# Kernel tuning notes

Measured on AMD Instinct MI355X. Metric: run time of the kernel, lower is better.

The kernel has to match this reference:

```python
import jax, jax.numpy as jnp
import numpy as np
from jax import lax

EPS = 1e-5  # BatchNorm eps (torch default)

def _up2_bilinear_ac(x):
    # bilinear upsample x2, align_corners=True; x: [B,C,H,W]
    B, C, H, W = x.shape
    def axis_interp(n_in, n_out):
        pos = jnp.arange(n_out, dtype=jnp.float32) * ((n_in - 1) / (n_out - 1))
        i0 = jnp.floor(pos).astype(jnp.int32)
        i1 = jnp.minimum(i0 + 1, n_in - 1)
        w = (pos - i0.astype(jnp.float32)).astype(x.dtype)
        return i0, i1, w
    i0, i1, wh = axis_interp(H, 2 * H)
    x = x[:, :, i0, :] * (1.0 - wh)[None, None, :, None] + x[:, :, i1, :] * wh[None, None, :, None]
    j0, j1, ww = axis_interp(W, 2 * W)
    x = x[:, :, :, j0] * (1.0 - ww) + x[:, :, :, j1] * ww
    return x

def setup_inputs() -> dict:
    key = jax.random.key(0)
    ks = jax.random.split(key, 8)
    B, Cin, Cout, H, W = 8, 64, 32, 128, 128
    att, K = 16, 2  # attention_channel = max(int(64*0.0625),16)=16; kernel_num=2
    n = lambda k, s, sc: jax.random.normal(k, s, jnp.float32) * sc
    return {
        'x': n(ks[0], (B, Cin, H, W), 1.0),
        'fc_w': n(ks[1], (att, Cin), 0.1),
        'bn_a_gamma': jnp.ones((att,), jnp.float32), 'bn_a_beta': jnp.zeros((att,), jnp.float32),
        'bn_a_mean': jnp.zeros((att,), jnp.float32), 'bn_a_var': jnp.ones((att,), jnp.float32),
        'ch_w': n(ks[2], (Cin, att), 0.1), 'ch_b': jnp.zeros((Cin,), jnp.float32),
        'fil_w': n(ks[3], (Cout, att), 0.1), 'fil_b': jnp.zeros((Cout,), jnp.float32),
        'sp_w': n(ks[4], (9, att), 0.1), 'sp_b': jnp.zeros((9,), jnp.float32),
        'k_w': n(ks[5], (K, att), 0.1), 'k_b': jnp.zeros((K,), jnp.float32),
        'weight': n(ks[6], (K, Cout, Cin, 3, 3), 0.05),
        'bn_gamma': jnp.ones((Cout,), jnp.float32), 'bn_beta': jnp.zeros((Cout,), jnp.float32),
        'bn_mean': jnp.zeros((Cout,), jnp.float32), 'bn_var': jnp.ones((Cout,), jnp.float32),
    }

def reference(x, fc_w, bn_a_gamma, bn_a_beta, bn_a_mean, bn_a_var,
              ch_w, ch_b, fil_w, fil_b, sp_w, sp_b, k_w, k_b,
              weight, bn_gamma, bn_beta, bn_mean, bn_var):
    x = _up2_bilinear_ac(x)
    B, Cin, H, W = x.shape
    K, Cout = weight.shape[0], weight.shape[1]
    # --- ODConv attention branch (on GAP features) ---
    g = x.mean(axis=(2, 3))                                    # [B,Cin]
    h = g @ fc_w.T                                             # [B,att]
    h = (h - bn_a_mean) / jnp.sqrt(bn_a_var + EPS) * bn_a_gamma + bn_a_beta
    h = jax.nn.relu(h)
    ch_att = jax.nn.sigmoid(h @ ch_w.T + ch_b)                 # [B,Cin]
    fil_att = jax.nn.sigmoid(h @ fil_w.T + fil_b)              # [B,Cout]
    sp_att = jax.nn.sigmoid(h @ sp_w.T + sp_b).reshape(B, 1, 1, 1, 3, 3)
    k_att = jax.nn.softmax(h @ k_w.T + k_b, axis=1).reshape(B, K, 1, 1, 1, 1)
    # per-sample aggregated filters: [B,Cout,Cin,3,3]
    agg_w = jnp.sum(k_att * sp_att * weight[None], axis=1)
    # --- dynamic conv (per-sample filter), channel-attended input ---
    x = x * ch_att[:, :, None, None]
    def conv1(xi, wi):
        return lax.conv_general_dilated(xi[None], wi, (1, 1), [(1, 1), (1, 1)],
                                        dimension_numbers=('NCHW', 'OIHW', 'NCHW'))[0]
    y = jax.vmap(conv1)(x, agg_w)                              # [B,Cout,H,W]
    y = y * fil_att[:, :, None, None]
    # --- BatchNorm2d (inference) + GELU (exact erf) ---
    y = (y - bn_mean[:, None, None]) / jnp.sqrt(bn_var[:, None, None] + EPS)
    y = y * bn_gamma[:, None, None] + bn_beta[:, None, None]
    return jax.nn.gelu(y, approximate=False)
```

## Files before the change

kernel.cpp:

```cpp
#include <hip/hip_runtime.h>
#include <hip/hip_bf16.h>

#define EPSBN 1e-5f

typedef short short8 __attribute__((ext_vector_type(8)));
typedef float f32x16 __attribute__((ext_vector_type(16)));

static __device__ __forceinline__ unsigned short f2u(float f){
  __hip_bfloat16 h = __float2bfloat16(f);
  union { __hip_bfloat16 h; unsigned short u; } c; c.h = h; return c.u;
}

#define WS_G     2048
#define WS_S     7168
#define WS_T     8192
#define WS_AGGB  16384
#define WS_XUP   327680

__global__ __launch_bounds__(256) void k_gap(const float* __restrict__ x, float* __restrict__ g){
  __shared__ float w[128];
  __shared__ float partial[4];
  int tid = threadIdx.x;
  if (tid < 128){
    int i = tid;
    float s = 0.f;
    int rstart = max(0, (int)floorf((float)(i-1)*(255.0f/127.0f)));
    #pragma unroll
    for (int k = 0; k < 8; ++k){
      int r = rstart + k;
      if (r <= 255){
        float pos = (float)r * (127.0f/255.0f);
        int i0 = (int)pos; float fr = pos - (float)i0; int i1 = min(i0+1,127);
        if (i0 == i) s += 1.0f - fr;
        if (i1 == i) s += fr;
      }
    }
    w[i] = s;
  }
  __syncthreads();
  const float4* xp = (const float4*)(x + ((size_t)blockIdx.x << 14));
  float s = 0.f;
  for (int gi = tid; gi < 4096; gi += 256){
    int i = gi >> 5, j4 = (gi & 31) * 4;
    float4 v = xp[gi];
    s += (v.x*w[j4] + v.y*w[j4+1] + v.z*w[j4+2] + v.w*w[j4+3]) * w[i];
  }
  for (int off = 32; off > 0; off >>= 1) s += __shfl_down(s, off, 64);
  if ((tid & 63) == 0) partial[tid >> 6] = s;
  __syncthreads();
  if (tid == 0) g[blockIdx.x] = (partial[0]+partial[1]+partial[2]+partial[3]) * (1.0f/65536.0f);
}

__global__ __launch_bounds__(256) void k_aggw(const float* __restrict__ g,
                      const float* __restrict__ fc_w,
                      const float* __restrict__ bga, const float* __restrict__ bba,
                      const float* __restrict__ bma, const float* __restrict__ bva,
                      const float* __restrict__ ch_w, const float* __restrict__ ch_b,
                      const float* __restrict__ fil_w, const float* __restrict__ fil_b,
                      const float* __restrict__ sp_w, const float* __restrict__ sp_b,
                      const float* __restrict__ k_w, const float* __restrict__ k_b,
                      const float* __restrict__ bn_g, const float* __restrict__ bn_b,
                      const float* __restrict__ bn_m, const float* __restrict__ bn_v,
                      const float* __restrict__ weight,
                      unsigned short* __restrict__ aggb,
                      float* __restrict__ sS, float* __restrict__ tT)
{
  __shared__ float h[8][16];
  int tid = threadIdx.x;
  if (tid < 128){
    int b = tid >> 4, a = tid & 15;
    float acc = 0.f;
    for (int c = 0; c < 64; ++c) acc += g[b*64+c] * fc_w[a*64+c];
    float v = (acc - bma[a]) * rsqrtf(bva[a] + EPSBN) * bga[a] + bba[a];
    h[b][a] = fmaxf(v, 0.f);
  }
  __syncthreads();

  int idx = blockIdx.x*256 + tid;
  int ci_l = idx & 31;
  int o    = (idx >> 5) & 31;
  int s    = (idx >> 10) % 9;
  int t2   = (idx >> 10) / 9;
  int cc   = t2 & 1, b = t2 >> 1;
  int ci   = cc*32 + ci_l;

  const float* hb = h[b];
  float zc = ch_b[ci], zs = sp_b[s];
  float z0 = k_b[0],  z1 = k_b[1];
  #pragma unroll
  for (int a = 0; a < 16; ++a){
    float hv = hb[a];
    zc += hv*ch_w[ci*16+a];
    zs += hv*sp_w[s*16+a];
    z0 += hv*k_w[a];
    z1 += hv*k_w[16+a];
  }
  float chv = 1.f/(1.f+expf(-zc));
  float spv = 1.f/(1.f+expf(-zs));
  float m = fmaxf(z0,z1);
  float e0 = expf(z0-m), e1 = expf(z1-m), inv = 1.f/(e0+e1);
  float ka0 = e0*inv, ka1 = e1*inv;
  float w0 = weight[(o*64+ci)*9+s];
  float w1 = weight[((32+o)*64+ci)*9+s];
  aggb[idx] = f2u(chv*spv*(ka0*w0 + ka1*w1));

  if (blockIdx.x == 0){
    int bb = tid >> 5, oo = tid & 31;
    float z = fil_b[oo];
    #pragma unroll
    for (int a = 0; a < 16; ++a) z += h[bb][a]*fil_w[oo*16+a];
    float f = 1.f/(1.f+expf(-z));
    float invs = rsqrtf(bn_v[oo] + EPSBN);
    sS[tid] = f * bn_g[oo] * invs;
    if (bb == 0) tT[oo] = bn_b[oo] - bn_m[oo]*bn_g[oo]*invs;
  }
}

__global__ __launch_bounds__(256) void k_up(const float* __restrict__ x,
                                            unsigned int* __restrict__ xup32)
{
  __shared__ float xin[16*798];
  int tid = threadIdx.x;
  int bi  = blockIdx.x;
  int strip = bi & 31, h16 = (bi >> 5) & 3, b = bi >> 7;
  int r0 = strip * 8;
  int i0b = (int)((float)r0 * (127.0f/255.0f));

  for (int e = tid; e < 12288; e += 256){
    int ir = e >> 11, rem = e & 2047, ci = rem >> 7, j = rem & 127;
    int row = min(i0b + ir, 127);
    xin[ci*798 + ir*133 + j] = x[(((size_t)(b*64 + h16*16 + ci)) << 14) + (row << 7) + j];
  }
  __syncthreads();

  int ci2 = tid & 7, cbase = tid >> 3;
  int j0t[8], j1t[8]; float wwt[8];
  #pragma unroll
  for (int jj = 0; jj < 8; ++jj){
    int c = cbase + 32*jj;
    float pos = (float)c * (127.0f/255.0f);
    int j0 = (int)pos;
    j0t[jj] = j0; j1t[jj] = min(j0+1,127); wwt[jj] = pos - (float)j0;
  }
  const float* base0 = &xin[(ci2*2+0)*798];
  const float* base1 = &xin[(ci2*2+1)*798];
  size_t pxbase = ((size_t)(b*2 + (h16>>1))) << 16;
  int halfoff = (h16 & 1)*8;

  for (int rr = 0; rr < 8; ++rr){
    int r = r0 + rr;
    float posr = (float)r * (127.0f/255.0f);
    int i0 = (int)posr; float wh = posr - (float)i0;
    int ir0 = (i0 - i0b)*133, ir1 = (min(i0+1,127) - i0b)*133;
    #pragma unroll
    for (int jj = 0; jj < 8; ++jj){
      int c = cbase + 32*jj;
      int j0 = j0t[jj], j1 = j1t[jj]; float ww = wwt[jj];
      float v00 = base0[ir0+j0], v01 = base0[ir0+j1];
      float v10 = base0[ir1+j0], v11 = base0[ir1+j1];
      float a0 = v00 + (v01-v00)*ww;
      float a1 = v10 + (v11-v10)*ww;
      float r0v = a0 + (a1-a0)*wh;
      float u00 = base1[ir0+j0], u01 = base1[ir0+j1];
      float u10 = base1[ir1+j0], u11 = base1[ir1+j1];
      float b0 = u00 + (u01-u00)*ww;
      float b1 = u10 + (u11-u10)*ww;
      float r1v = b0 + (b1-b0)*wh;
      unsigned pack = (unsigned)f2u(r0v) | (((unsigned)f2u(r1v)) << 16);
      xup32[(pxbase + (size_t)(r*256 + c))*16 + halfoff + ci2] = pack;
    }
  }
}

#define XT_STRIDE 40
__global__ __launch_bounds__(256) void k_conv(const unsigned short* __restrict__ xup,
                                              const unsigned short* __restrict__ aggb,
                                              const float* __restrict__ sS,
                                              const float* __restrict__ tT,
                                              float* __restrict__ out)
{
  __shared__ unsigned short xt[18*18*XT_STRIDE];
  __shared__ unsigned short wt[288*XT_STRIDE];
  __shared__ float sSs[32], tTs[32];

  int tid = threadIdx.x;
  int bi  = blockIdx.x;
  int b   = bi >> 8, t = bi & 255;
  int p0  = (t >> 4) * 16, q0 = (t & 15) * 16;
  int lane = tid & 63, wv = tid >> 6;
  if (tid < 32){ sSs[tid] = sS[b*32+tid]; tTs[tid] = tT[tid]; }

  int ldsoff[6], gmoff[6]; bool val[6];
  int cnt = (tid < 16) ? 6 : 5;
  for (int k = 0; k < cnt; ++k){
    int e = tid + (k << 8);
    int rr = e / 72; int rem = e - rr*72; int qq = rem >> 2; int gq4 = rem & 3;
    int gr = p0 - 1 + rr, gq = q0 - 1 + qq;
    val[k]    = ((unsigned)gr < 256u) && ((unsigned)gq < 256u);
    ldsoff[k] = (rr*18+qq)*XT_STRIDE + gq4*8;
    gmoff[k]  = (gr*256+gq)*32 + gq4*8;
  }

  f32x16 acc[2];
  #pragma unroll
  for (int i = 0; i < 16; ++i){ acc[0][i] = 0.f; acc[1][i] = 0.f; }

  int n  = lane & 31;
  int kq = lane >> 5;

  for (int cc = 0; cc < 2; ++cc){
    if (cc) __syncthreads();
    const unsigned short* xb = xup + (((size_t)(b*2+cc)) << 21);
    for (int k = 0; k < cnt; ++k){
      short8 v = {0,0,0,0,0,0,0,0};
      if (val[k]) v = *(const short8*)&xb[gmoff[k]];
      *(short8*)&xt[ldsoff[k]] = v;
    }
    const unsigned short* wbg = aggb + ((size_t)(b*2+cc))*9216;
    for (int e = tid; e < 1152; e += 256){
      *(short8*)&wt[(e >> 2)*XT_STRIDE + (e & 3)*8] = *(const short8*)&wbg[e*8];
    }
    __syncthreads();

    #pragma unroll
    for (int s = 0; s < 9; ++s){
      const int ky = s / 3, kx = s % 3;
      #pragma unroll
      for (int k2 = 0; k2 < 2; ++k2){
        short8 av = *(const short8*)&wt[(s*32 + n)*XT_STRIDE + k2*16 + kq*8];
        #pragma unroll
        for (int tt = 0; tt < 2; ++tt){
          int lr = 2*(2*wv + tt) + (n >> 4);
          int rr = lr + ky;
          int qq = (n & 15) + kx;
          short8 bv = *(const short8*)&xt[(rr*18+qq)*XT_STRIDE + k2*16 + kq*8];
          acc[tt] = __builtin_amdgcn_mfma_f32_32x32x16_bf16(av, bv, acc[tt], 0, 0, 0);
        }
      }
    }
  }

  #pragma unroll
  for (int tt = 0; tt < 2; ++tt){
    int lr = 2*(2*wv + tt) + (n >> 4);
    int p = p0 + lr, q = q0 + (n & 15);
    #pragma unroll
    for (int r = 0; r < 16; ++r){
      int o = (r & 3) + 8*(r >> 2) + 4*kq;
      float valv = acc[tt][r]*sSs[o] + tTs[o];
      float gl  = 0.5f*valv*(1.f + erff(valv*0.70710678118f));
      out[(((size_t)(b*32+o)) << 16) + (p << 8) + q] = gl;
    }
  }
}

extern "C" void kernel_launch(void* const* d_in, const int* in_sizes, int n_in,
                              void* d_out, int out_size, void* d_ws, size_t ws_size,
                              hipStream_t stream)
{
  const float* x     = (const float*)d_in[0];
  const float* fc_w  = (const float*)d_in[1];
  const float* bga   = (const float*)d_in[2];
  const float* bba   = (const float*)d_in[3];
  const float* bma   = (const float*)d_in[4];
  const float* bva   = (const float*)d_in[5];
  const float* ch_w  = (const float*)d_in[6];
  const float* ch_b  = (const float*)d_in[7];
  const float* fil_w = (const float*)d_in[8];
  const float* fil_b = (const float*)d_in[9];
  const float* sp_w  = (const float*)d_in[10];
  const float* sp_b  = (const float*)d_in[11];
  const float* k_w   = (const float*)d_in[12];
  const float* k_b   = (const float*)d_in[13];
  const float* weight= (const float*)d_in[14];
  const float* bn_g  = (const float*)d_in[15];
  const float* bn_b  = (const float*)d_in[16];
  const float* bn_m  = (const float*)d_in[17];
  const float* bn_v  = (const float*)d_in[18];

  char* ws = (char*)d_ws;
  float* g   = (float*)(ws + WS_G);
  float* sS  = (float*)(ws + WS_S);
  float* tT  = (float*)(ws + WS_T);
  unsigned short* aggb = (unsigned short*)(ws + WS_AGGB);
  unsigned short* xup  = (unsigned short*)(ws + WS_XUP);
  float* out = (float*)d_out;

  hipLaunchKernelGGL(k_gap,  dim3(512),  dim3(256), 0, stream, x, g);
  hipLaunchKernelGGL(k_aggw, dim3(576),  dim3(256), 0, stream, g, fc_w, bga, bba, bma, bva,
                     ch_w, ch_b, fil_w, fil_b, sp_w, sp_b, k_w, k_b,
                     bn_g, bn_b, bn_m, bn_v, weight, aggb, sS, tT);
  hipLaunchKernelGGL(k_up,   dim3(1024), dim3(256), 0, stream, x, (unsigned int*)xup);
  hipLaunchKernelGGL(k_conv, dim3(2048), dim3(256), 0, stream, xup, aggb, sS, tT, out);
}
```

Before: 206.8 us.

## Split upsampled activations into 16-channel planes and load conv weights directly from global

The upsample kernel now writes activations as four 8-pair (16-channel) planes per sample, and the conv kernel's LDS tile fill reads from these planes. The conv kernel no longer stages the aggregated weights in shared memory. Each wave reads its MFMA A operands straight from global memory (likely L2-resident), which removes the weight LDS buffer and its fill traffic. A launch bound of five blocks per CU is added to raise occupancy, at the cost of more global loads inside the MFMA loop and tighter register limits.

Result: slower. 255.3 us (+23.5%).

```diff
diff --git a/kernel.cpp b/kernel.cpp
--- a/kernel.cpp
+++ b/kernel.cpp
@@ -144,8 +144,7 @@
   }
   const float* base0 = &xin[(ci2*2+0)*798];
   const float* base1 = &xin[(ci2*2+1)*798];
-  size_t pxbase = ((size_t)(b*2 + (h16>>1))) << 16;
-  int halfoff = (h16 & 1)*8;
+  size_t plane32 = ((size_t)(b*4 + h16)) << 19;
 
   for (int rr = 0; rr < 8; ++rr){
     int r = r0 + rr;
@@ -167,20 +166,19 @@
       float b1 = u10 + (u11-u10)*ww;
       float r1v = b0 + (b1-b0)*wh;
       unsigned pack = (unsigned)f2u(r0v) | (((unsigned)f2u(r1v)) << 16);
-      xup32[(pxbase + (size_t)(r*256 + c))*16 + halfoff + ci2] = pack;
+      xup32[plane32 + (size_t)(r*256 + c)*8 + ci2] = pack;
     }
   }
 }
 
 #define XT_STRIDE 40
-__global__ __launch_bounds__(256) void k_conv(const unsigned short* __restrict__ xup,
+__global__ __launch_bounds__(256, 5) void k_conv(const unsigned short* __restrict__ xup,
                                               const unsigned short* __restrict__ aggb,
                                               const float* __restrict__ sS,
                                               const float* __restrict__ tT,
                                               float* __restrict__ out)
 {
   __shared__ unsigned short xt[18*18*XT_STRIDE];
-  __shared__ unsigned short wt[288*XT_STRIDE];
   __shared__ float sSs[32], tTs[32];
 
   int tid = threadIdx.x;
@@ -190,15 +188,16 @@
   int lane = tid & 63, wv = tid >> 6;
   if (tid < 32){ sSs[tid] = sS[b*32+tid]; tTs[tid] = tT[tid]; }
 
-  int ldsoff[6], gmoff[6]; bool val[6];
+  int ldsoff[6], pmoff[6]; bool val[6];
   int cnt = (tid < 16) ? 6 : 5;
   for (int k = 0; k < cnt; ++k){
     int e = tid + (k << 8);
-    int rr = e / 72; int rem = e - rr*72; int qq = rem >> 2; int gq4 = rem & 3;
+    int rr = e / 72; int rem = e - rr*72;
+    int qq = rem >> 2; int k2 = (rem >> 1) & 1; int kq = rem & 1;
     int gr = p0 - 1 + rr, gq = q0 - 1 + qq;
     val[k]    = ((unsigned)gr < 256u) && ((unsigned)gq < 256u);
-    ldsoff[k] = (rr*18+qq)*XT_STRIDE + gq4*8;
-    gmoff[k]  = (gr*256+gq)*32 + gq4*8;
+    ldsoff[k] = (rr*18+qq)*XT_STRIDE + k2*16 + kq*8;
+    pmoff[k]  = (k2 << 20) + (gr*256+gq)*16 + kq*8;
   }
 
   f32x16 acc[2];
@@ -210,32 +209,32 @@
 
   for (int cc = 0; cc < 2; ++cc){
     if (cc) __syncthreads();
-    const unsigned short* xb = xup + (((size_t)(b*2+cc)) << 21);
+    const unsigned short* xb = xup + (((size_t)(b*4 + 2*cc)) << 20);
     for (int k = 0; k < cnt; ++k){
       short8 v = {0,0,0,0,0,0,0,0};
-      if (val[k]) v = *(const short8*)&xb[gmoff[k]];
+      if (val[k]) v = *(const short8*)&xb[pmoff[k]];
       *(short8*)&xt[ldsoff[k]] = v;
     }
-    const unsigned short* wbg = aggb + ((size_t)(b*2+cc))*9216;
-    for (int e = tid; e < 1152; e += 256){
-      *(short8*)&wt[(e >> 2)*XT_STRIDE + (e & 3)*8] = *(const short8*)&wbg[e*8];
-    }
     __syncthreads();
+
+    const unsigned short* ab = aggb + (((size_t)(b*2+cc))*9*32 + n)*32 + kq*8;
 
     #pragma unroll
     for (int s = 0; s < 9; ++s){
       const int ky = s / 3, kx = s % 3;
+      const unsigned short* ap = ab + s*1024;
+      short8 av0 = *(const short8*)&ap[0];
+      short8 av1 = *(const short8*)&ap[16];
       #pragma unroll
-      for (int k2 = 0; k2 < 2; ++k2){
-        short8 av = *(const short8*)&wt[(s*32 + n)*XT_STRIDE + k2*16 + kq*8];
-        #pragma unroll
-        for (int tt = 0; tt < 2; ++tt){
-          int lr = 2*(2*wv + tt) + (n >> 4);
-          int rr = lr + ky;
-          int qq = (n & 15) + kx;
-          short8 bv = *(const short8*)&xt[(rr*18+qq)*XT_STRIDE + k2*16 + kq*8];
-          acc[tt] = __builtin_amdgcn_mfma_f32_32x32x16_bf16(av, bv, acc[tt], 0, 0, 0);
-        }
+      for (int tt = 0; tt < 2; ++tt){
+        int lr = 2*(2*wv + tt) + (n >> 4);
+        int rr = lr + ky;
+        int qq = (n & 15) + kx;
+        const unsigned short* xrow = &xt[(rr*18+qq)*XT_STRIDE + kq*8];
+        short8 bv0 = *(const short8*)&xrow[0];
+        short8 bv1 = *(const short8*)&xrow[16];
+        acc[tt] = __builtin_amdgcn_mfma_f32_32x32x16_bf16(av0, bv0, acc[tt], 0, 0, 0);
+        acc[tt] = __builtin_amdgcn_mfma_f32_32x32x16_bf16(av1, bv1, acc[tt], 0, 0, 0);
       }
     }
   }
```
